# Optimization experiments

Hardware: AMD Instinct MI355X
Metric: run time of the kernel (lower is better)

Reference implementation:

```python
import jax, jax.numpy as jnp
import numpy as np

B = 256      # batch
D = 31       # per-mode feature dim (before bias-1 column)
FUSED = (D + 1) ** 3  # 32768
H1, H2, NCLS = 1024, 256, 4


def setup_inputs() -> dict:
    key = jax.random.key(0)
    ks = jax.random.split(key, 9)
    s = lambda fan_in: 1.0 / np.sqrt(fan_in)
    return {
        "x0": jax.random.normal(ks[0], (B, D), dtype=jnp.float32),
        "x1": jax.random.normal(ks[1], (B, D), dtype=jnp.float32),
        "x2": jax.random.normal(ks[2], (B, D), dtype=jnp.float32),
        "W1": jax.random.uniform(ks[3], (FUSED, H1), jnp.float32, -s(FUSED), s(FUSED)),
        "b1": jax.random.uniform(ks[4], (H1,), jnp.float32, -s(FUSED), s(FUSED)),
        "W2": jax.random.uniform(ks[5], (H1, H2), jnp.float32, -s(H1), s(H1)),
        "b2": jax.random.uniform(ks[6], (H2,), jnp.float32, -s(H1), s(H1)),
        "W3": jax.random.uniform(ks[7], (H2, NCLS), jnp.float32, -s(H2), s(H2)),
        "b3": jax.random.uniform(ks[8], (NCLS,), jnp.float32, -s(H2), s(H2)),
    }


def reference(x0, x1, x2, W1, b1, W2, b2, W3, b3):
    ones = jnp.ones((x0.shape[0], 1), dtype=x0.dtype)
    z0 = jnp.concatenate([x0, ones], axis=1)  # [B, D+1]
    z1 = jnp.concatenate([x1, ones], axis=1)
    z2 = jnp.concatenate([x2, ones], axis=1)
    # Batched triple outer product (vectorized over B, replacing the per-sample loop)
    fused = jnp.einsum("bi,bj,bk->bijk", z0, z1, z2).reshape(x0.shape[0], -1)  # [B, (D+1)^3]
    h = jax.nn.relu(fused @ W1 + b1)
    h = jax.nn.relu(h @ W2 + b2)
    return h @ W3 + b3  # [B, NCLS]
```

## Files before the change

kernel.cpp:

```cpp
#include <hip/hip_runtime.h>


typedef _Float16 half8 __attribute__((ext_vector_type(8)));
typedef _Float16 half4 __attribute__((ext_vector_type(4)));
typedef _Float16 half2 __attribute__((ext_vector_type(2)));
typedef float f32x4 __attribute__((ext_vector_type(4)));

#define KSPLIT 16

__global__ __launch_bounds__(512, 4) void k1_gemm(
    const float* __restrict__ x0, const float* __restrict__ x1,
    const float* __restrict__ x2, const float* __restrict__ W1,
    float* __restrict__ partial)
{
    constexpr int GRPS = 16;
    __shared__ __align__(16) _Float16 z01L[GRPS][256][4];
    __shared__ __align__(16) _Float16 tile[4][1024];

    const int tid  = threadIdx.x;
    const int nt   = blockIdx.x & 31;
    const int ks   = blockIdx.x >> 5;
    const int lane = tid & 63;
    const int w    = tid >> 6;
    const int nl   = lane & 15;
    const int g    = lane >> 4;
    const int kbase = ks * 2048;
    const int n0    = nt * 32;

    {
        const int b  = tid & 255;
        const int hf = tid >> 8;
        const int i  = ks * 2 + hf;
        const float v0 = (i < 31) ? x0[b * 31 + i] : 1.0f;
#pragma unroll
        for (int pp = 0; pp < 32; pp += 4) {
            half4 hv;
#pragma unroll
            for (int e = 0; e < 4; ++e) {
                int j = pp + e;
                float v1 = (j < 31) ? x1[b * 31 + j] : 1.0f;
                hv[e] = (_Float16)(v0 * v1);
            }
            *(half4*)&z01L[(hf * 32 + pp) >> 2][b][0] = hv;
        }
    }

    half8 z2v[2];
#pragma unroll
    for (int ms = 0; ms < 2; ++ms) {
        int b = w * 32 + ms * 16 + nl;
#pragma unroll
        for (int e = 0; e < 8; ++e) {
            int kp = g * 8 + e;
            z2v[ms][e] = (_Float16)((kp < 31) ? x2[b * 31 + kp] : 1.0f);
        }
    }

    const int sn  = tid & 31;
    const int sk2 = tid >> 5;
    const float* gsrc = W1 + (size_t)(kbase + sk2 * 2) * 1024 + n0 + sn;
    const int wswz = (((sn & 7) ^ (sn >> 3)) & 7) << 2;
    const int woff = sn * 32 + ((sk2 * 2) ^ wswz);

    int roff[2][2];
#pragma unroll
    for (int ns = 0; ns < 2; ++ns) {
        int n = ns * 16 + nl;
        int s = (((n & 7) ^ (n >> 3)) & 7) << 2;
        roff[ns][0] = n * 32 + ((g * 8) ^ s);
        roff[ns][1] = n * 32 + ((g * 8 + 4) ^ s);
    }

    __syncthreads();

    float rxv[4], ryv[4];
#pragma unroll
    for (int s = 0; s < 4; ++s) {
        rxv[s] = gsrc[(size_t)s * 32768];
        ryv[s] = gsrc[(size_t)s * 32768 + 1024];
    }
    {
        half2 hv; hv[0] = (_Float16)rxv[0]; hv[1] = (_Float16)ryv[0];
        *(half2*)&tile[0][woff] = hv;
    }
    asm volatile("s_waitcnt lgkmcnt(0)\n\ts_barrier" ::: "memory");

    f32x4 acc[2][2] = {};
    half4 zq0, zq1;

#define ITER(T_, TT, ISSUE, WRITE)                                             \
    {                                                                          \
        if (ISSUE) {                                                           \
            rxv[TT] = gsrc[(size_t)((T_) + 4) * 32768];                        \
            ryv[TT] = gsrc[(size_t)((T_) + 4) * 32768 + 1024];                 \
        }                                                                      \
        if ((TT) == 0) {                                                       \
            zq0 = *(const half4*)&z01L[(T_) >> 2][w * 32 + nl][0];             \
            zq1 = *(const half4*)&z01L[(T_) >> 2][w * 32 + 16 + nl][0];        \
        }                                                                      \
        const _Float16* tb = &tile[(T_) & 3][0];                               \
        half4 lo0 = *(const half4*)&tb[roff[0][0]];                            \
        half4 hi0 = *(const half4*)&tb[roff[0][1]];                            \
        half4 lo1 = *(const half4*)&tb[roff[1][0]];                            \
        half4 hi1 = *(const half4*)&tb[roff[1][1]];                            \
        half8 bh0 = __builtin_shufflevector(lo0, hi0, 0,1,2,3,4,5,6,7);        \
        half8 bh1 = __builtin_shufflevector(lo1, hi1, 0,1,2,3,4,5,6,7);        \
        half8 a0 = z2v[0] * zq0[TT];                                           \
        half8 a1 = z2v[1] * zq1[TT];                                           \
        acc[0][0] = __builtin_amdgcn_mfma_f32_16x16x32_f16(a0, bh0, acc[0][0], 0, 0, 0); \
        acc[0][1] = __builtin_amdgcn_mfma_f32_16x16x32_f16(a0, bh1, acc[0][1], 0, 0, 0); \
        acc[1][0] = __builtin_amdgcn_mfma_f32_16x16x32_f16(a1, bh0, acc[1][0], 0, 0, 0); \
        acc[1][1] = __builtin_amdgcn_mfma_f32_16x16x32_f16(a1, bh1, acc[1][1], 0, 0, 0); \
        if (WRITE) {                                                           \
            half2 hv;                                                          \
            hv[0] = (_Float16)rxv[((TT) + 1) & 3];                             \
            hv[1] = (_Float16)ryv[((TT) + 1) & 3];                             \
            *(half2*)&tile[((T_) + 1) & 3][woff] = hv;                         \
        }                                                                      \
        asm volatile("s_waitcnt lgkmcnt(0)\n\ts_barrier" ::: "memory");        \
    }

    for (int grp = 0; grp < 15; ++grp) {
        const int t = grp * 4;
        ITER(t + 0, 0, 1, 1)
        ITER(t + 1, 1, 1, 1)
        ITER(t + 2, 2, 1, 1)
        ITER(t + 3, 3, 1, 1)
    }
    ITER(60, 0, 0, 1)
    ITER(61, 1, 0, 1)
    ITER(62, 2, 0, 1)
    ITER(63, 3, 0, 0)
#undef ITER

    float* pout = partial + (size_t)ks * (256 * 1024);
#pragma unroll
    for (int ms = 0; ms < 2; ++ms)
#pragma unroll
        for (int ns = 0; ns < 2; ++ns)
#pragma unroll
            for (int r = 0; r < 4; ++r) {
                int brow = w * 32 + ms * 16 + g * 4 + r;
                int ncol = n0 + ns * 16 + nl;
                pout[brow * 1024 + ncol] = acc[ms][ns][r];
            }
}

__global__ __launch_bounds__(256) void k2_reduce(
    const float* __restrict__ partial, const float* __restrict__ b1,
    float* __restrict__ h1)
{
    int e = blockIdx.x * 256 + threadIdx.x;
    float s = 0.f;
#pragma unroll
    for (int sp = 0; sp < KSPLIT; ++sp) s += partial[(size_t)sp * 262144 + e];
    s += b1[e & 1023];
    h1[e] = fmaxf(s, 0.f);
}

__global__ __launch_bounds__(256) void k3_layer2(
    const float* __restrict__ h1, const float* __restrict__ W2,
    float* __restrict__ p2)
{
    __shared__ float h1t[32 * 129];
    __shared__ float w2t[128 * 65];
    const int tid = threadIdx.x;
    const int m0 = blockIdx.x * 32, n0 = blockIdx.y * 64, k0 = blockIdx.z * 128;

    for (int idx = tid; idx < 32 * 128; idx += 256) {
        int m = idx >> 7, kk = idx & 127;
        h1t[m * 129 + kk] = h1[(m0 + m) * 1024 + k0 + kk];
    }
    for (int idx = tid; idx < 128 * 64; idx += 256) {
        int kk = idx >> 6, n = idx & 63;
        w2t[kk * 65 + n] = W2[(k0 + kk) * 256 + n0 + n];
    }
    __syncthreads();

    const int tn = tid & 63, tm = tid >> 6;
    float acc[8] = {};
    for (int kk = 0; kk < 128; ++kk) {
        float w = w2t[kk * 65 + tn];
#pragma unroll
        for (int r = 0; r < 8; ++r)
            acc[r] += h1t[(tm * 8 + r) * 129 + kk] * w;
    }
#pragma unroll
    for (int r = 0; r < 8; ++r)
        p2[blockIdx.z * 65536 + (m0 + tm * 8 + r) * 256 + n0 + tn] = acc[r];
}

__global__ __launch_bounds__(256) void k4_final(
    const float* __restrict__ p2, const float* __restrict__ b2,
    const float* __restrict__ W3, const float* __restrict__ b3,
    float* __restrict__ out)
{
    __shared__ float pL[256 * 5];
    const int b = blockIdx.x, n = threadIdx.x;
    float s = 0.f;
#pragma unroll
    for (int sp = 0; sp < 8; ++sp) s += p2[sp * 65536 + b * 256 + n];
    float h2 = fmaxf(s + b2[n], 0.f);
#pragma unroll
    for (int c = 0; c < 4; ++c) pL[n * 5 + c] = h2 * W3[n * 4 + c];
    __syncthreads();

    const int lane = n & 63, w = n >> 6;
    float v = pL[lane * 5 + w] + pL[(lane + 64) * 5 + w] +
              pL[(lane + 128) * 5 + w] + pL[(lane + 192) * 5 + w];
#pragma unroll
    for (int off = 32; off > 0; off >>= 1) v += __shfl_down(v, off);
    if (lane == 0) out[b * 4 + w] = v + b3[w];
}

extern "C" void kernel_launch(void* const* d_in, const int* in_sizes, int n_in,
                              void* d_out, int out_size, void* d_ws, size_t ws_size,
                              hipStream_t stream)
{
    (void)in_sizes; (void)n_in; (void)out_size; (void)ws_size;
    const float* x0 = (const float*)d_in[0];
    const float* x1 = (const float*)d_in[1];
    const float* x2 = (const float*)d_in[2];
    const float* W1 = (const float*)d_in[3];
    const float* b1 = (const float*)d_in[4];
    const float* W2 = (const float*)d_in[5];
    const float* b2 = (const float*)d_in[6];
    const float* W3 = (const float*)d_in[7];
    const float* b3 = (const float*)d_in[8];
    float* out = (float*)d_out;
    float* ws  = (float*)d_ws;

    float* partial = ws;
    float* h1 = ws;
    float* p2 = ws + 262144;

    k1_gemm  <<<dim3(512),     dim3(512), 0, stream>>>(x0, x1, x2, W1, partial);
    k2_reduce<<<dim3(1024),    dim3(256), 0, stream>>>(partial, b1, h1);
    k3_layer2<<<dim3(8, 4, 8), dim3(256), 0, stream>>>(h1, W2, p2);
    k4_final <<<dim3(256),     dim3(256), 0, stream>>>(p2, b2, W3, b3, out);
}
```

Measured before the change: 51.92 us.

## Store split-K partials and h1 in fp16, enlarge layer-2 M tile

```diff
diff --git a/kernel.cpp b/kernel.cpp
--- a/kernel.cpp
+++ b/kernel.cpp
@@ -11,7 +11,7 @@
 __global__ __launch_bounds__(512, 4) void k1_gemm(
     const float* __restrict__ x0, const float* __restrict__ x1,
     const float* __restrict__ x2, const float* __restrict__ W1,
-    float* __restrict__ partial)
+    _Float16* __restrict__ partial)
 {
     constexpr int GRPS = 16;
     __shared__ __align__(16) _Float16 z01L[GRPS][256][4];
@@ -133,7 +133,7 @@
     ITER(63, 3, 0, 0)
 #undef ITER
 
-    float* pout = partial + (size_t)ks * (256 * 1024);
+    _Float16* pout = partial + ((size_t)ks << 18);
 #pragma unroll
     for (int ms = 0; ms < 2; ++ms)
 #pragma unroll
@@ -142,34 +142,41 @@
             for (int r = 0; r < 4; ++r) {
                 int brow = w * 32 + ms * 16 + g * 4 + r;
                 int ncol = n0 + ns * 16 + nl;
-                pout[brow * 1024 + ncol] = acc[ms][ns][r];
+                pout[brow * 1024 + ncol] = (_Float16)acc[ms][ns][r];
             }
 }
 
 __global__ __launch_bounds__(256) void k2_reduce(
-    const float* __restrict__ partial, const float* __restrict__ b1,
-    float* __restrict__ h1)
-{
-    int e = blockIdx.x * 256 + threadIdx.x;
-    float s = 0.f;
-#pragma unroll
-    for (int sp = 0; sp < KSPLIT; ++sp) s += partial[(size_t)sp * 262144 + e];
-    s += b1[e & 1023];
-    h1[e] = fmaxf(s, 0.f);
+    const _Float16* __restrict__ partial, const float* __restrict__ b1,
+    _Float16* __restrict__ h1)
+{
+    int e2 = blockIdx.x * 256 + threadIdx.x;
+    const half2* pv = (const half2*)partial;
+    float s0 = 0.f, s1 = 0.f;
+#pragma unroll
+    for (int sp = 0; sp < KSPLIT; ++sp) {
+        half2 v = pv[(size_t)sp * 131072 + e2];
+        s0 += (float)v[0]; s1 += (float)v[1];
+    }
+    int h = (e2 * 2) & 1023;
+    half2 o;
+    o[0] = (_Float16)fmaxf(s0 + b1[h], 0.f);
+    o[1] = (_Float16)fmaxf(s1 + b1[h + 1], 0.f);
+    ((half2*)h1)[e2] = o;
 }
 
 __global__ __launch_bounds__(256) void k3_layer2(
-    const float* __restrict__ h1, const float* __restrict__ W2,
+    const _Float16* __restrict__ h1, const float* __restrict__ W2,
     float* __restrict__ p2)
 {
-    __shared__ float h1t[32 * 129];
+    __shared__ float h1t[64 * 129];
     __shared__ float w2t[128 * 65];
     const int tid = threadIdx.x;
-    const int m0 = blockIdx.x * 32, n0 = blockIdx.y * 64, k0 = blockIdx.z * 128;
-
-    for (int idx = tid; idx < 32 * 128; idx += 256) {
+    const int m0 = blockIdx.x * 64, n0 = blockIdx.y * 64, k0 = blockIdx.z * 128;
+
+    for (int idx = tid; idx < 64 * 128; idx += 256) {
         int m = idx >> 7, kk = idx & 127;
-        h1t[m * 129 + kk] = h1[(m0 + m) * 1024 + k0 + kk];
+        h1t[m * 129 + kk] = (float)h1[(m0 + m) * 1024 + k0 + kk];
     }
     for (int idx = tid; idx < 128 * 64; idx += 256) {
         int kk = idx >> 6, n = idx & 63;
@@ -178,16 +185,16 @@
     __syncthreads();
 
     const int tn = tid & 63, tm = tid >> 6;
-    float acc[8] = {};
+    float acc[16] = {};
     for (int kk = 0; kk < 128; ++kk) {
-        float w = w2t[kk * 65 + tn];
-#pragma unroll
-        for (int r = 0; r < 8; ++r)
-            acc[r] += h1t[(tm * 8 + r) * 129 + kk] * w;
-    }
-#pragma unroll
-    for (int r = 0; r < 8; ++r)
-        p2[blockIdx.z * 65536 + (m0 + tm * 8 + r) * 256 + n0 + tn] = acc[r];
+        float wv = w2t[kk * 65 + tn];
+#pragma unroll
+        for (int r = 0; r < 16; ++r)
+            acc[r] += h1t[(tm * 16 + r) * 129 + kk] * wv;
+    }
+#pragma unroll
+    for (int r = 0; r < 16; ++r)
+        p2[blockIdx.z * 65536 + (m0 + tm * 16 + r) * 256 + n0 + tn] = acc[r];
 }
 
 __global__ __launch_bounds__(256) void k4_final(
@@ -202,7 +209,7 @@
     for (int sp = 0; sp < 8; ++sp) s += p2[sp * 65536 + b * 256 + n];
     float h2 = fmaxf(s + b2[n], 0.f);
 #pragma unroll
-    for (int c = 0; c < 4; ++c) pL[n * 5 + c] = h2 * W3[n * 4 + c];
+    for (int ccls = 0; ccls < 4; ++ccls) pL[n * 5 + ccls] = h2 * W3[n * 4 + ccls];
     __syncthreads();
 
     const int lane = n & 63, w = n >> 6;
@@ -228,14 +235,13 @@
     const float* W3 = (const float*)d_in[7];
     const float* b3 = (const float*)d_in[8];
     float* out = (float*)d_out;
-    float* ws  = (float*)d_ws;
-
-    float* partial = ws;
-    float* h1 = ws;
-    float* p2 = ws + 262144;
+
+    _Float16* partial = (_Float16*)d_ws;
+    _Float16* h1 = (_Float16*)((char*)d_ws + (size_t)KSPLIT * 262144 * 2);
+    float* p2 = (float*)((char*)h1 + 262144 * 2);
 
     k1_gemm  <<<dim3(512),     dim3(512), 0, stream>>>(x0, x1, x2, W1, partial);
-    k2_reduce<<<dim3(1024),    dim3(256), 0, stream>>>(partial, b1, h1);
-    k3_layer2<<<dim3(8, 4, 8), dim3(256), 0, stream>>>(h1, W2, p2);
+    k2_reduce<<<dim3(512),     dim3(256), 0, stream>>>(partial, b1, h1);
+    k3_layer2<<<dim3(4, 4, 8), dim3(256), 0, stream>>>(h1, W2, p2);
     k4_final <<<dim3(256),     dim3(256), 0, stream>>>(p2, b2, W3, b3, out);
 }
```

Measured after the change: 54.98 us. +5.9%, slower.
